# Performance work log

Hardware: AMD Instinct MI355X
Metric: run time of the kernel (lower is better)

The kernel has to match this reference:

```python
import jax, jax.numpy as jnp
import numpy as np

N_HEAD = 16
D_MODEL = 1024
MAX_LEN = 1024  # must equal D_MODEL for the original module's final conv to typecheck
B = 8
L = 1024


def _conv1x1(x, W, b):
    # Conv1d kernel_size=1: [B, C_in, L] -> [B, C_out, L]
    return jnp.einsum('oc,bcl->bol', W, x) + b[None, :, None]


def setup_inputs() -> dict:
    key = jax.random.key(0)
    ks = jax.random.split(key, 11)
    s = 0.02
    return {
        'q': jax.random.normal(ks[0], (B, D_MODEL, L), jnp.float32),
        'k': jax.random.normal(ks[1], (B, D_MODEL, L), jnp.float32),
        'v': jax.random.normal(ks[2], (B, D_MODEL, L), jnp.float32),
        'Wq': jax.random.normal(ks[3], (MAX_LEN, D_MODEL), jnp.float32) * s,
        'bq': jnp.zeros((MAX_LEN,), jnp.float32),
        'Wk': jax.random.normal(ks[4], (MAX_LEN, D_MODEL), jnp.float32) * s,
        'bk': jnp.zeros((MAX_LEN,), jnp.float32),
        'Wv': jax.random.normal(ks[5], (MAX_LEN, D_MODEL), jnp.float32) * s,
        'bv': jnp.zeros((MAX_LEN,), jnp.float32),
        'Wo': jax.random.normal(ks[6], (D_MODEL, D_MODEL), jnp.float32) * s,
        'bo': jnp.zeros((D_MODEL,), jnp.float32),
    }


def reference(q, k, v, Wq, bq, Wk, bk, Wv, bv, Wo, bo):
    # 1x1-conv projections: [B, d_model, L] -> [B, max_len, L]
    qp = _conv1x1(q, Wq, bq)
    kp = _conv1x1(k, Wk, bk)
    vp = _conv1x1(v, Wv, bv)

    b_, ml, l = qp.shape
    dt = l // N_HEAD  # d_tensor
    # project(): raw view splitting the LAST axis blockwise (no transpose!)
    qh = qp.reshape(b_, N_HEAD, ml, dt)
    kh = kp.reshape(b_, N_HEAD, ml, dt)
    vh = vp.reshape(b_, N_HEAD, ml, dt)

    # ScaleDotProductAttention: k_t is a raw VIEW to [b, h, dt, ml], not a transpose
    k_t = kh.reshape(b_, N_HEAD, dt, ml)
    score = jnp.matmul(qh, k_t) / jnp.sqrt(jnp.float32(dt))  # [b, h, ml, ml]
    # nn.Softmax() with dim=None on a 4D tensor -> softmax over dim=1 (legacy torch)
    score = jax.nn.softmax(score, axis=1)
    out = jnp.matmul(score, vh)  # [b, h, ml, dt]

    # concat(): raw view back to [b, ml, l]
    out = out.reshape(b_, ml, l)
    # final 1x1 conv (requires ml == d_model)
    return _conv1x1(out, Wo, bo)
```

## Files before the change

kernel.cpp:

```cpp
#include <hip/hip_runtime.h>
#include <hip/hip_bf16.h>
#include <cstdint>

using bf16 = __hip_bfloat16;
typedef __bf16 bf16x8 __attribute__((ext_vector_type(8)));
typedef float f32x4 __attribute__((ext_vector_type(4)));

#define DEV static __device__ __forceinline__

DEV float toF(float x) { return x; }
DEV float toF(bf16 x) { return __bfloat162float(x); }

DEV float lo2f(unsigned int u) { return __builtin_bit_cast(float, u << 16); }
DEV float hi2f(unsigned int u) { return __builtin_bit_cast(float, u & 0xffff0000u); }
DEV unsigned int pkr(float lo, float hi) {
  return ((__builtin_bit_cast(unsigned int, lo) + 0x8000u) >> 16) |
         ((__builtin_bit_cast(unsigned int, hi) + 0x8000u) & 0xffff0000u);
}
DEV float fexp2(float x) {
  float r;
  asm("v_exp_f32 %0, %1" : "=v"(r) : "v"(x));
  return r;
}
DEV float frcp(float x) {
  float r;
  asm("v_rcp_f32 %0, %1" : "=v"(r) : "v"(x));
  return r;
}

DEV void gload_lds16(const void* g, void* l) {
  __builtin_amdgcn_global_load_lds(
      (const __attribute__((address_space(1))) unsigned int*)g,
      (__attribute__((address_space(3))) unsigned int*)l, 16, 0, 0);
}

#define GEMM_CORE(A_, lda_, B_, ldb_)                                          \
  f32x4 acc[4][2] = {};                                                        \
  {                                                                            \
    const int wave = tid >> 6, lane = tid & 63;                                \
    const int wm = (wave >> 1) * 64, wn = (wave & 1) * 32;                     \
    const int lrow = lane & 15;                                                \
    const int g = lane >> 4;                                                   \
    const int xk = lrow & 7;                                                   \
    for (int k0 = 0; k0 < 1024; k0 += 64) {                                    \
      _Pragma("unroll") for (int r = 0; r < 4; ++r) {                          \
        int c = r * 256 + tid;                                                 \
        int row = c >> 3, sub = c & 7;                                         \
        gload_lds16(A_ + (long long)(m0 + row) * lda_ + k0 +                   \
                        ((sub ^ (row & 7)) << 3),                              \
                    (void*)(ldsA + (r * 256 + wave * 64) * 8));                \
      }                                                                        \
      _Pragma("unroll") for (int r = 0; r < 2; ++r) {                          \
        int c = r * 256 + tid;                                                 \
        int row = c >> 3, sub = c & 7;                                         \
        gload_lds16(B_ + (long long)(n0 + row) * ldb_ + k0 +                   \
                        ((sub ^ (row & 7)) << 3),                              \
                    (void*)(ldsB + (r * 256 + wave * 64) * 8));                \
      }                                                                        \
      __syncthreads();                                                         \
      _Pragma("unroll") for (int kc = 0; kc < 2; ++kc) {                       \
        bf16x8 af[4], bfr[2];                                                  \
        _Pragma("unroll") for (int i = 0; i < 4; ++i)                          \
            af[i] = *(const bf16x8*)&ldsA[(wm + i * 16 + lrow) * 64 +          \
                                          (((kc * 4 + g) ^ xk) << 3)];         \
        _Pragma("unroll") for (int j = 0; j < 2; ++j)                          \
            bfr[j] = *(const bf16x8*)&ldsB[(wn + j * 16 + lrow) * 64 +         \
                                           (((kc * 4 + g) ^ xk) << 3)];        \
        _Pragma("unroll") for (int i = 0; i < 4; ++i)                          \
            _Pragma("unroll") for (int j = 0; j < 2; ++j)                      \
                acc[i][j] = __builtin_amdgcn_mfma_f32_16x16x32_bf16(           \
                    af[i], bfr[j], acc[i][j], 0, 0, 0);                        \
      }                                                                        \
      __syncthreads();                                                         \
    }                                                                          \
  }

__launch_bounds__(256, 4)
__global__ void proj3(const bf16* __restrict__ Wq, const bf16* __restrict__ qT,
                      bf16* __restrict__ qp, const float* __restrict__ bq,
                      const bf16* __restrict__ kT, const bf16* __restrict__ Wk,
                      bf16* __restrict__ kph, const float* __restrict__ bk,
                      const bf16* __restrict__ Wv, const bf16* __restrict__ vT,
                      bf16* __restrict__ vptc, const float* __restrict__ bv) {
  __shared__ bf16 ldsA[128 * 64];
  __shared__ bf16 ldsB[64 * 64];
  const int tid = threadIdx.x;
  const int bid = blockIdx.x;
  const int which = bid >> 10, r0b = bid & 1023;
  const long long z = r0b & 7;
  const int t = r0b >> 3;
  const int m0 = (t >> 4) * 128, n0 = (t & 15) * 64;
  const long long M1 = 1048576;

  const bf16* A;
  const bf16* B;
  const float* bias;
  bf16* C;
  float alpha;
  if (which == 0) {
    A = Wq; B = qT + z * M1; bias = bq; C = qp + z * M1; alpha = 0.18033688f;
  } else if (which == 1) {
    A = kT + z * M1; B = Wk; bias = bk; C = kph + z * M1; alpha = 1.0f;
  } else {
    A = Wv; B = vT + z * M1; bias = bv; C = vptc + z * M1; alpha = 1.0f;
  }

  GEMM_CORE(A, 1024, B, 1024)

  const int wave = tid >> 6, lane = tid & 63;
  const int wm = (wave >> 1) * 64, wn = (wave & 1) * 32;
  const int lrow = lane & 15;
  const int r4 = (lane >> 4) * 4;
#pragma unroll
  for (int i = 0; i < 4; ++i) {
#pragma unroll
    for (int j = 0; j < 2; ++j) {
#pragma unroll
      for (int r = 0; r < 4; ++r) {
        int grow = m0 + wm + i * 16 + r4 + r;
        int gcol = n0 + wn + j * 16 + lrow;
        float vv = acc[i][j][r];
        if (which == 0) {
          vv = (vv + bias[grow]) * alpha;
          C[(long long)grow * 1024 + gcol] = __float2bfloat16(vv);
        } else if (which == 1) {
          vv += bias[gcol];
          long long idx = ((long long)(gcol >> 6) << 16) + grow * 64 + (gcol & 63);
          C[idx] = __float2bfloat16(vv);
        } else {
          vv += bias[grow];
          int mm = ((grow & 63) << 4) | (gcol >> 6);
          long long idx = ((long long)(grow >> 6) << 16) + ((mm >> 5) << 11) +
                          ((gcol & 63) << 5) + (mm & 31);
          C[idx] = __float2bfloat16(vv);
        }
      }
    }
  }
}

__launch_bounds__(256, 4)
__global__ void gemm_out(const bf16* __restrict__ Wo, const bf16* __restrict__ aoutT,
                         float* __restrict__ out, const float* __restrict__ bo) {
  __shared__ bf16 ldsA[128 * 64];
  __shared__ bf16 ldsB[64 * 64];
  const int tid = threadIdx.x;
  const int bid = blockIdx.x;
  const long long z = bid & 7;
  const int t = bid >> 3;
  const int m0 = (t >> 4) * 128, n0 = (t & 15) * 64;
  const long long M1 = 1048576;
  const bf16* A = Wo;
  const bf16* B = aoutT + z * M1;
  float* C = out + z * M1;

  GEMM_CORE(A, 1024, B, 1024)

  const int wave = tid >> 6, lane = tid & 63;
  const int wm = (wave >> 1) * 64, wn = (wave & 1) * 32;
  const int lrow = lane & 15;
  const int r4 = (lane >> 4) * 4;
#pragma unroll
  for (int i = 0; i < 4; ++i)
#pragma unroll
    for (int j = 0; j < 2; ++j)
#pragma unroll
      for (int r = 0; r < 4; ++r) {
        int grow = m0 + wm + i * 16 + r4 + r;
        int gcol = n0 + wn + j * 16 + lrow;
        C[(long long)grow * 1024 + gcol] = acc[i][j][r] + bo[grow];
      }
}

__launch_bounds__(1024, 4)
__global__ void fused_attn(const bf16* __restrict__ qp,
                           const bf16* __restrict__ kph,
                           const bf16* __restrict__ vptc,
                           bf16* __restrict__ aout) {
  __shared__ unsigned int SP[16 * 32 * 68];
  const int bid = blockIdx.x;
  const int bb = bid & 7, mt = bid >> 3;
  const int tid = threadIdx.x;
  const int w = tid >> 6, lane = tid & 63;
  const int l15 = lane & 15, g = lane >> 4;

  const bf16* Qb = qp + ((size_t)bb << 20);
  const bf16* Kb = kph + ((size_t)bb << 20) + ((size_t)w << 16);
  const bf16* Vb = vptc + ((size_t)bb << 20) + ((size_t)w << 16);
  bf16* Ob = aout + ((size_t)bb << 20);

  bf16x8 qf[2][2];
#pragma unroll
  for (int mf = 0; mf < 2; ++mf)
#pragma unroll
    for (int kc = 0; kc < 2; ++kc)
      qf[mf][kc] = *(const bf16x8*)(Qb + ((size_t)w << 16) +
                                    (mt * 32 + mf * 16 + l15) * 64 + kc * 32 + g * 8);

  f32x4 oacc[2][4] = {};
  const unsigned int hrow = w * 2176;

  for (int it = 0; it < 8; ++it) {
    const int n0 = it * 128;
#pragma unroll
    for (int mmf = 0; mmf < 8; ++mmf) {
      const bf16* kr = Kb + (size_t)(n0 + mmf * 16 + l15) * 64 + g * 8;
      bf16x8 k0 = *(const bf16x8*)kr;
      bf16x8 k1 = *(const bf16x8*)(kr + 32);
      f32x4 sa = {}, sb = {};
      __builtin_amdgcn_s_setprio(1);
      sa = __builtin_amdgcn_mfma_f32_16x16x32_bf16(k0, qf[0][0], sa, 0, 0, 0);
      sa = __builtin_amdgcn_mfma_f32_16x16x32_bf16(k1, qf[0][1], sa, 0, 0, 0);
      sb = __builtin_amdgcn_mfma_f32_16x16x32_bf16(k0, qf[1][0], sb, 0, 0, 0);
      sb = __builtin_amdgcn_mfma_f32_16x16x32_bf16(k1, qf[1][1], sb, 0, 0, 0);
      __builtin_amdgcn_s_setprio(0);
      uint2 ua, ub;
      ua.x = pkr(sa[0], sa[1]);
      ua.y = pkr(sa[2], sa[3]);
      ub.x = pkr(sb[0], sb[1]);
      ub.y = pkr(sb[2], sb[3]);
      *(uint2*)&SP[hrow + l15 * 68 + mmf * 8 + g * 2] = ua;
      *(uint2*)&SP[hrow + (16 + l15) * 68 + mmf * 8 + g * 2] = ub;
    }
    __syncthreads();
#pragma unroll
    for (int pi = 0; pi < 2; ++pi) {
      const int p = tid + pi * 1024;
      const int base = (p >> 6) * 68 + (p & 63);
      float el[16], eh[16];
#pragma unroll
      for (int h = 0; h < 16; ++h) {
        unsigned int u = SP[h * 2176 + base];
        el[h] = fexp2(lo2f(u));
        eh[h] = fexp2(hi2f(u));
      }
      float sl = (((el[0] + el[1]) + (el[2] + el[3])) + ((el[4] + el[5]) + (el[6] + el[7]))) +
                 (((el[8] + el[9]) + (el[10] + el[11])) + ((el[12] + el[13]) + (el[14] + el[15])));
      float sh = (((eh[0] + eh[1]) + (eh[2] + eh[3])) + ((eh[4] + eh[5]) + (eh[6] + eh[7]))) +
                 (((eh[8] + eh[9]) + (eh[10] + eh[11])) + ((eh[12] + eh[13]) + (eh[14] + eh[15])));
      float il = frcp(sl), ih = frcp(sh);
#pragma unroll
      for (int h = 0; h < 16; ++h)
        SP[h * 2176 + base] = pkr(el[h] * il, eh[h] * ih);
    }
    __syncthreads();
#pragma unroll
    for (int c = 0; c < 4; ++c) {
      uint4 pa0 = *(const uint4*)&SP[hrow + l15 * 68 + c * 16 + g * 4];
      uint4 pa1 = *(const uint4*)&SP[hrow + (16 + l15) * 68 + c * 16 + g * 4];
      bf16x8 p0 = __builtin_bit_cast(bf16x8, pa0);
      bf16x8 p1 = __builtin_bit_cast(bf16x8, pa1);
      const bf16* vb = Vb + ((it * 4 + c) << 11) + g * 8;
      __builtin_amdgcn_s_setprio(1);
#pragma unroll
      for (int dj = 0; dj < 4; ++dj) {
        bf16x8 vf = *(const bf16x8*)(vb + (dj * 16 + l15) * 32);
        oacc[0][dj] = __builtin_amdgcn_mfma_f32_16x16x32_bf16(p0, vf, oacc[0][dj], 0, 0, 0);
        oacc[1][dj] = __builtin_amdgcn_mfma_f32_16x16x32_bf16(p1, vf, oacc[1][dj], 0, 0, 0);
      }
      __builtin_amdgcn_s_setprio(0);
    }
  }
#pragma unroll
  for (int mf = 0; mf < 2; ++mf)
#pragma unroll
    for (int dj = 0; dj < 4; ++dj)
#pragma unroll
      for (int r = 0; r < 4; ++r)
        Ob[((size_t)w << 16) + (size_t)(mt * 32 + mf * 16 + g * 4 + r) * 64 +
           dj * 16 + l15] = __float2bfloat16(oacc[mf][dj][r]);
}

template <typename TIN>
__global__ void transpose_tile(const TIN* __restrict__ in, bf16* __restrict__ out,
                               int R, int C, long long sIn, long long sOut) {
  __shared__ float t[32][33];
  const long long z = blockIdx.z;
  in += z * sIn;
  out += z * sOut;
  const int r0 = blockIdx.y * 32, c0 = blockIdx.x * 32;
  const int tx = threadIdx.x, ty = threadIdx.y;
#pragma unroll
  for (int i = ty; i < 32; i += 8)
    t[i][tx] = toF(in[(long long)(r0 + i) * C + c0 + tx]);
  __syncthreads();
#pragma unroll
  for (int i = ty; i < 32; i += 8)
    out[(long long)(c0 + i) * R + r0 + tx] = __float2bfloat16(t[tx][i]);
}

__global__ void transpose_in3(const float* __restrict__ q, const float* __restrict__ k,
                              const float* __restrict__ v, bf16* __restrict__ qT,
                              bf16* __restrict__ kT, bf16* __restrict__ vT) {
  __shared__ float t[32][33];
  const int z = blockIdx.z, bz = z & 7, which = z >> 3;
  const float* in = (which == 0 ? q : which == 1 ? k : v) + (size_t)bz * 1048576;
  bf16* out = (which == 0 ? qT : which == 1 ? kT : vT) + (size_t)bz * 1048576;
  const int r0 = blockIdx.y * 32, c0 = blockIdx.x * 32;
  const int tx = threadIdx.x, ty = threadIdx.y;
#pragma unroll
  for (int i = ty; i < 32; i += 8)
    t[i][tx] = in[(size_t)(r0 + i) * 1024 + c0 + tx];
  __syncthreads();
#pragma unroll
  for (int i = ty; i < 32; i += 8)
    out[(size_t)(c0 + i) * 1024 + r0 + tx] = __float2bfloat16(t[tx][i]);
}

__global__ void cast4(const float* __restrict__ w0, const float* __restrict__ w1,
                      const float* __restrict__ w2, const float* __restrict__ w3,
                      bf16* __restrict__ o0, bf16* __restrict__ o1,
                      bf16* __restrict__ o2, bf16* __restrict__ o3) {
  const int y = blockIdx.y;
  const float* in = y == 0 ? w0 : y == 1 ? w1 : y == 2 ? w2 : w3;
  bf16* out = y == 0 ? o0 : y == 1 ? o1 : y == 2 ? o2 : o3;
  int i = (blockIdx.x * 256 + threadIdx.x) * 4;
  float4 f = *(const float4*)(in + i);
  out[i + 0] = __float2bfloat16(f.x);
  out[i + 1] = __float2bfloat16(f.y);
  out[i + 2] = __float2bfloat16(f.z);
  out[i + 3] = __float2bfloat16(f.w);
}

extern "C" void kernel_launch(void* const* d_in, const int* in_sizes, int n_in,
                              void* d_out, int out_size, void* d_ws, size_t ws_size,
                              hipStream_t stream) {
  (void)in_sizes; (void)n_in; (void)out_size;
  const float* q  = (const float*)d_in[0];
  const float* k  = (const float*)d_in[1];
  const float* v  = (const float*)d_in[2];
  const float* Wq = (const float*)d_in[3];
  const float* bq = (const float*)d_in[4];
  const float* Wk = (const float*)d_in[5];
  const float* bk = (const float*)d_in[6];
  const float* Wv = (const float*)d_in[7];
  const float* bv = (const float*)d_in[8];
  const float* Wo = (const float*)d_in[9];
  const float* bo = (const float*)d_in[10];
  float* out = (float*)d_out;

  const size_t MB = 1ull << 20;
  if (ws_size < 152 * MB) return;
  char* ws = (char*)d_ws;
  bf16* qp    = (bf16*)(ws + 0 * MB);
  bf16* kph   = (bf16*)(ws + 16 * MB);
  bf16* vptc  = (bf16*)(ws + 32 * MB);
  bf16* aout  = (bf16*)(ws + 48 * MB);
  bf16* aoutT = (bf16*)(ws + 64 * MB);
  bf16* WoB   = (bf16*)(ws + 80 * MB);
  char* scr = ws + 82 * MB;
  bf16* WqB = (bf16*)(scr + 0 * MB);
  bf16* WkB = (bf16*)(scr + 2 * MB);
  bf16* WvB = (bf16*)(scr + 4 * MB);
  bf16* qT  = (bf16*)(scr + 6 * MB);
  bf16* kT  = (bf16*)(scr + 22 * MB);
  bf16* vT  = (bf16*)(scr + 38 * MB);

  const long long M1 = 1048576;
  dim3 tb(32, 8);

  cast4<<<dim3(1024, 4), 256, 0, stream>>>(Wq, Wk, Wv, Wo, WqB, WkB, WvB, WoB);
  transpose_in3<<<dim3(32, 32, 24), tb, 0, stream>>>(q, k, v, qT, kT, vT);
  proj3<<<3072, 256, 0, stream>>>(WqB, qT, qp, bq, kT, WkB, kph, bk, WvB, vT, vptc, bv);

  fused_attn<<<dim3(256), 1024, 0, stream>>>(qp, kph, vptc, aout);

  transpose_tile<bf16><<<dim3(32, 32, 8), tb, 0, stream>>>(aout, aoutT, 1024, 1024, M1, M1);
  gemm_out<<<1024, 256, 0, stream>>>(WoB, aoutT, out, bo);
}
```

Baseline: 299.8 us.

## Double-buffer score tiles and overlap next QK chunk with current softmax

The attention loop now works on 64-column chunks over 16 iterations instead of 128-column chunks over 8, with two shared-memory buffers. The QK^T MFMAs for the next chunk are issued before the cross-head softmax of the current chunk, so matrix and exp/reduction work can overlap. This drops one block-wide barrier per chunk. The row stride is reduced to 35 words to fit both buffers, which leaves the vector LDS accesses only 4-byte aligned and may cause unaligned or split LDS transactions.

```diff
diff --git a/kernel.cpp b/kernel.cpp
--- a/kernel.cpp
+++ b/kernel.cpp
@@ -172,12 +172,36 @@
       }
 }
 
+#define QK_CHUNK(itv, SPn)                                                     \
+  {                                                                            \
+    const int mm0 = (itv) * 64;                                                \
+    _Pragma("unroll") for (int mmf = 0; mmf < 4; ++mmf) {                      \
+      const bf16* kr = Kb + (size_t)(mm0 + mmf * 16 + l15) * 64 + g * 8;       \
+      bf16x8 k0 = *(const bf16x8*)kr;                                          \
+      bf16x8 k1 = *(const bf16x8*)(kr + 32);                                   \
+      f32x4 sa = {}, sb = {};                                                  \
+      __builtin_amdgcn_s_setprio(1);                                           \
+      sa = __builtin_amdgcn_mfma_f32_16x16x32_bf16(k0, qf[0][0], sa, 0, 0, 0); \
+      sa = __builtin_amdgcn_mfma_f32_16x16x32_bf16(k1, qf[0][1], sa, 0, 0, 0); \
+      sb = __builtin_amdgcn_mfma_f32_16x16x32_bf16(k0, qf[1][0], sb, 0, 0, 0); \
+      sb = __builtin_amdgcn_mfma_f32_16x16x32_bf16(k1, qf[1][1], sb, 0, 0, 0); \
+      __builtin_amdgcn_s_setprio(0);                                           \
+      uint2 ua, ub;                                                            \
+      ua.x = pkr(sa[0], sa[1]);                                                \
+      ua.y = pkr(sa[2], sa[3]);                                                \
+      ub.x = pkr(sb[0], sb[1]);                                                \
+      ub.y = pkr(sb[2], sb[3]);                                                \
+      *(uint2*)&(SPn)[hrow + l15 * 35 + mmf * 8 + g * 2] = ua;                 \
+      *(uint2*)&(SPn)[hrow + (16 + l15) * 35 + mmf * 8 + g * 2] = ub;          \
+    }                                                                          \
+  }
+
 __launch_bounds__(1024, 4)
 __global__ void fused_attn(const bf16* __restrict__ qp,
                            const bf16* __restrict__ kph,
                            const bf16* __restrict__ vptc,
                            bf16* __restrict__ aout) {
-  __shared__ unsigned int SP[16 * 32 * 68];
+  __shared__ unsigned int SP[2][16 * 32 * 35];
   const int bid = blockIdx.x;
   const int bb = bid & 7, mt = bid >> 3;
   const int tid = threadIdx.x;
@@ -198,39 +222,20 @@
                                     (mt * 32 + mf * 16 + l15) * 64 + kc * 32 + g * 8);
 
   f32x4 oacc[2][4] = {};
-  const unsigned int hrow = w * 2176;
-
-  for (int it = 0; it < 8; ++it) {
-    const int n0 = it * 128;
-#pragma unroll
-    for (int mmf = 0; mmf < 8; ++mmf) {
-      const bf16* kr = Kb + (size_t)(n0 + mmf * 16 + l15) * 64 + g * 8;
-      bf16x8 k0 = *(const bf16x8*)kr;
-      bf16x8 k1 = *(const bf16x8*)(kr + 32);
-      f32x4 sa = {}, sb = {};
-      __builtin_amdgcn_s_setprio(1);
-      sa = __builtin_amdgcn_mfma_f32_16x16x32_bf16(k0, qf[0][0], sa, 0, 0, 0);
-      sa = __builtin_amdgcn_mfma_f32_16x16x32_bf16(k1, qf[0][1], sa, 0, 0, 0);
-      sb = __builtin_amdgcn_mfma_f32_16x16x32_bf16(k0, qf[1][0], sb, 0, 0, 0);
-      sb = __builtin_amdgcn_mfma_f32_16x16x32_bf16(k1, qf[1][1], sb, 0, 0, 0);
-      __builtin_amdgcn_s_setprio(0);
-      uint2 ua, ub;
-      ua.x = pkr(sa[0], sa[1]);
-      ua.y = pkr(sa[2], sa[3]);
-      ub.x = pkr(sb[0], sb[1]);
-      ub.y = pkr(sb[2], sb[3]);
-      *(uint2*)&SP[hrow + l15 * 68 + mmf * 8 + g * 2] = ua;
-      *(uint2*)&SP[hrow + (16 + l15) * 68 + mmf * 8 + g * 2] = ub;
-    }
-    __syncthreads();
-#pragma unroll
-    for (int pi = 0; pi < 2; ++pi) {
-      const int p = tid + pi * 1024;
-      const int base = (p >> 6) * 68 + (p & 63);
+  const unsigned int hrow = w * 1120;
+  const int smbase = (tid >> 5) * 35 + (tid & 31);
+
+  QK_CHUNK(0, SP[0])
+  __syncthreads();
+
+  for (int it = 0; it < 16; ++it) {
+    unsigned int* SPc = SP[it & 1];
+    if (it < 15) QK_CHUNK(it + 1, SP[(it + 1) & 1])
+    {
       float el[16], eh[16];
 #pragma unroll
       for (int h = 0; h < 16; ++h) {
-        unsigned int u = SP[h * 2176 + base];
+        unsigned int u = SPc[h * 1120 + smbase];
         el[h] = fexp2(lo2f(u));
         eh[h] = fexp2(hi2f(u));
       }
@@ -241,16 +246,16 @@
       float il = frcp(sl), ih = frcp(sh);
 #pragma unroll
       for (int h = 0; h < 16; ++h)
-        SP[h * 2176 + base] = pkr(el[h] * il, eh[h] * ih);
+        SPc[h * 1120 + smbase] = pkr(el[h] * il, eh[h] * ih);
     }
     __syncthreads();
 #pragma unroll
-    for (int c = 0; c < 4; ++c) {
-      uint4 pa0 = *(const uint4*)&SP[hrow + l15 * 68 + c * 16 + g * 4];
-      uint4 pa1 = *(const uint4*)&SP[hrow + (16 + l15) * 68 + c * 16 + g * 4];
+    for (int c = 0; c < 2; ++c) {
+      uint4 pa0 = *(const uint4*)&SPc[hrow + l15 * 35 + c * 16 + g * 4];
+      uint4 pa1 = *(const uint4*)&SPc[hrow + (16 + l15) * 35 + c * 16 + g * 4];
       bf16x8 p0 = __builtin_bit_cast(bf16x8, pa0);
       bf16x8 p1 = __builtin_bit_cast(bf16x8, pa1);
-      const bf16* vb = Vb + ((it * 4 + c) << 11) + g * 8;
+      const bf16* vb = Vb + ((it * 2 + c) << 11) + g * 8;
       __builtin_amdgcn_s_setprio(1);
 #pragma unroll
       for (int dj = 0; dj < 4; ++dj) {
```

Result: faster. 292.4 us (-2.5%).
